# Optimization experiments

Hardware: AMD Instinct MI355X
Metric: run time of the kernel (lower is better)

Reference implementation:

```python
import jax, jax.numpy as jnp
import numpy as np

N = 100000  # nodes
E = 1600000  # edges
F = 128      # nfeat == nclass (source constructs every layer as nfeat->nclass)


def setup_inputs() -> dict:
    key = jax.random.key(0)
    ks = jax.random.split(key, 8)
    x = jax.random.normal(ks[0], (N, F), dtype=jnp.float32)
    row = jax.random.randint(ks[1], (E,), 0, N)
    col = jax.random.randint(ks[2], (E,), 0, N)
    s = (1.0 / np.sqrt(F)).astype(np.float32) if hasattr(1.0/np.sqrt(F), 'astype') else 1.0/np.sqrt(F)
    s = 1.0 / np.sqrt(F)
    W0 = jax.random.uniform(ks[3], (F, F), jnp.float32, -s, s)
    b0 = jax.random.uniform(ks[4], (F,), jnp.float32, -s, s)
    W1 = jax.random.uniform(ks[5], (F, F), jnp.float32, -s, s)
    b1 = jax.random.uniform(ks[6], (F,), jnp.float32, -s, s)
    return {"x": x, "W0": W0, "b0": b0, "W1": W1, "b1": b1, "row": row, "col": col}


def _gcn_layer(h_in, W, b, row, col, dinv):
    # h = Linear(feat)
    h = h_in @ W + b
    # (D^-1/2 (A+I) D^-1/2) @ h, A in COO (row=i, col=j), A[i,j]=1
    coef = dinv[row] * dinv[col]                      # [E]
    msg = h[col] * coef[:, None]                       # [E, F] gather
    agg = jax.ops.segment_sum(msg, row, num_segments=N)
    agg = agg + (dinv * dinv)[:, None] * h             # self loops (identity)
    return agg


def reference(x, W0, b0, W1, b1, row, col):
    # D_hat = diag((A + I).sum(0)) -> column sums + 1
    deg = jax.ops.segment_sum(jnp.ones((E,), jnp.float32), col, num_segments=N) + 1.0
    dinv = deg ** -0.5
    h = _gcn_layer(x, W0, b0, row, col, dinv)
    h = jax.nn.relu(h)            # with_relu=True; dropout off (eval mode)
    h = _gcn_layer(h, W1, b1, row, col, dinv)
    return jax.nn.log_softmax(h, axis=1)
```

## Files before the change

kernel.cpp:

```cpp
#include <hip/hip_runtime.h>
#include <math.h>

#define FDIM 128
#define RPB 128
#define BSTRIDE 32
#define NBLK 256
#define MAXB 1024

typedef __attribute__((ext_vector_type(8))) short short8;
typedef __attribute__((ext_vector_type(4))) float floatx4;

static __device__ __forceinline__ unsigned short f2bf(float f) {
    unsigned int u = __float_as_uint(f);
    u = (u + 0x7fff + ((u >> 16) & 1)) >> 16;
    return (unsigned short)u;
}

static __device__ __forceinline__ void bf2f(unsigned int u, float& a, float& b) {
    a = __uint_as_float(u << 16);
    b = __uint_as_float(u & 0xffff0000u);
}


__global__ __launch_bounds__(256) void k_zero(int* rbCnt, int* cbCnt, int nbs) {
    int i = blockIdx.x * 256 + threadIdx.x;
    if (i < nbs) { rbCnt[i] = 0; cbCnt[i] = 0; }
}

__global__ __launch_bounds__(256) void k_count(const int* __restrict__ row, const int* __restrict__ col,
                                               int* rbCnt, int* cbCnt, int nE, int nb) {
    __shared__ int rh[MAXB];
    __shared__ int ch[MAXB];
    const int tid = threadIdx.x;
    const int cpb = (nE + NBLK - 1) / NBLK;
    const int e0 = blockIdx.x * cpb;
    int e1 = e0 + cpb; if (e1 > nE) e1 = nE;
    for (int i = tid; i < nb; i += 256) { rh[i] = 0; ch[i] = 0; }
    __syncthreads();
    for (int e = e0 + tid; e < e1; e += 256) {
        atomicAdd(&rh[row[e] >> 7], 1);
        atomicAdd(&ch[col[e] >> 7], 1);
    }
    __syncthreads();
    for (int i = tid; i < nb; i += 256) {
        if (rh[i]) atomicAdd(&rbCnt[(size_t)i * BSTRIDE], rh[i]);
        if (ch[i]) atomicAdd(&cbCnt[(size_t)i * BSTRIDE], ch[i]);
    }
}

__global__ __launch_bounds__(1024) void k_bscan(const int* __restrict__ rbCnt, const int* __restrict__ cbCnt,
                                                int* rbBase, int* cbBase, int* rbCur, int* cbCur,
                                                int nb, int nE) {
    __shared__ int s[1024];
    int tid = threadIdx.x;
    int v = (tid < nb) ? rbCnt[(size_t)tid * BSTRIDE] : 0;
    s[tid] = v;
    __syncthreads();
    for (int off = 1; off < 1024; off <<= 1) {
        int t = (tid >= off) ? s[tid - off] : 0;
        __syncthreads();
        s[tid] += t;
        __syncthreads();
    }
    if (tid < nb) {
        int ex = s[tid] - v;
        rbBase[tid] = ex;
        rbCur[(size_t)tid * BSTRIDE] = ex;
    }
    if (tid == 0) rbBase[nb] = nE;
    __syncthreads();
    v = (tid < nb) ? cbCnt[(size_t)tid * BSTRIDE] : 0;
    s[tid] = v;
    __syncthreads();
    for (int off = 1; off < 1024; off <<= 1) {
        int t = (tid >= off) ? s[tid - off] : 0;
        __syncthreads();
        s[tid] += t;
        __syncthreads();
    }
    if (tid < nb) {
        int ex = s[tid] - v;
        cbBase[tid] = ex;
        cbCur[(size_t)tid * BSTRIDE] = ex;
    }
    if (tid == 0) cbBase[nb] = nE;
}

__global__ __launch_bounds__(256) void k_scatter2(const int* __restrict__ row, const int* __restrict__ col,
                                                  int* rbCur, int* cbCur,
                                                  unsigned int* __restrict__ pairs,
                                                  unsigned char* __restrict__ clocal, int nE, int nb) {
    __shared__ int rh[MAXB];
    __shared__ int ch[MAXB];
    __shared__ int rbase[MAXB];
    __shared__ int cbase[MAXB];
    const int tid = threadIdx.x;
    const int cpb = (nE + NBLK - 1) / NBLK;
    const int e0 = blockIdx.x * cpb;
    int e1 = e0 + cpb; if (e1 > nE) e1 = nE;

    for (int i = tid; i < nb; i += 256) { rh[i] = 0; ch[i] = 0; }
    __syncthreads();
    for (int e = e0 + tid; e < e1; e += 256) {
        atomicAdd(&rh[row[e] >> 7], 1);
        atomicAdd(&ch[col[e] >> 7], 1);
    }
    __syncthreads();
    for (int i = tid; i < nb; i += 256) {
        rbase[i] = rh[i] ? atomicAdd(&rbCur[(size_t)i * BSTRIDE], rh[i]) : 0;
        cbase[i] = ch[i] ? atomicAdd(&cbCur[(size_t)i * BSTRIDE], ch[i]) : 0;
        rh[i] = 0;
        ch[i] = 0;
    }
    __syncthreads();
    for (int e = e0 + tid; e < e1; e += 256) {
        int r = row[e];
        int c = col[e];
        int rb = r >> 7, cb = c >> 7;
        int p = rbase[rb] + atomicAdd(&rh[rb], 1);
        pairs[p] = ((unsigned int)(r & (RPB - 1)) << 25) | (unsigned int)c;
        int q = cbase[cb] + atomicAdd(&ch[cb], 1);
        clocal[q] = (unsigned char)(c & (RPB - 1));
    }
}

__global__ __launch_bounds__(256) void k_rowsort(const int* __restrict__ rbBase,
                                                 const unsigned int* __restrict__ pairs,
                                                 int* __restrict__ row_ptr, int* __restrict__ csr_col,
                                                 int n, int nb) {
    __shared__ int hist[RPB];
    __shared__ int scan[RPB];
    __shared__ int lcur[RPB];
    const int b = blockIdx.x;
    const int tid = threadIdx.x;
    const int row0 = b * RPB;
    const int start = rbBase[b];
    const int endp = rbBase[b + 1];

    if (tid < RPB) hist[tid] = 0;
    __syncthreads();
    for (int i = start + tid; i < endp; i += 256)
        atomicAdd(&hist[pairs[i] >> 25], 1);
    __syncthreads();

    if (tid < RPB) scan[tid] = hist[tid];
    __syncthreads();
    for (int off = 1; off < RPB; off <<= 1) {
        int t = (tid < RPB && tid >= off) ? scan[tid - off] : 0;
        __syncthreads();
        if (tid < RPB) scan[tid] += t;
        __syncthreads();
    }
    if (tid < RPB) {
        int ex = start + scan[tid] - hist[tid];
        lcur[tid] = ex;
        int r = row0 + tid;
        if (r < n) row_ptr[r] = ex;
    }
    if (b == nb - 1 && tid == 0) row_ptr[n] = endp;
    __syncthreads();

    for (int i = start + tid; i < endp; i += 256) {
        unsigned int u = pairs[i];
        int pos = atomicAdd(&lcur[u >> 25], 1);
        csr_col[pos] = (int)(u & 0x1FFFFFFu);
    }
}

__global__ __launch_bounds__(256) void k_colhist(const int* __restrict__ cbBase,
                                                 const unsigned char* __restrict__ clocal,
                                                 float* __restrict__ dinv, int n) {
    __shared__ int hist[RPB];
    const int b = blockIdx.x;
    const int tid = threadIdx.x;
    const int start = cbBase[b];
    const int endp = cbBase[b + 1];
    if (tid < RPB) hist[tid] = 0;
    __syncthreads();
    for (int i = start + tid; i < endp; i += 256)
        atomicAdd(&hist[(int)clocal[i]], 1);
    __syncthreads();
    if (tid < RPB) {
        int c = b * RPB + tid;
        if (c < n) dinv[c] = rsqrtf((float)hist[tid] + 1.0f);
    }
}


__global__ __launch_bounds__(256) void k_cvt(const float2* __restrict__ x, unsigned int* __restrict__ xb,
                                             int total) {
    int i = blockIdx.x * 256 + threadIdx.x;
    if (i < total) {
        float2 v = x[i];
        xb[i] = (unsigned int)f2bf(v.x) | ((unsigned int)f2bf(v.y) << 16);
    }
}

__global__ __launch_bounds__(256) void k_cvtW(const float* __restrict__ W0, const float* __restrict__ W1,
                                              unsigned short* __restrict__ W0t, unsigned short* __restrict__ W1t) {
    const float* W = blockIdx.x ? W1 : W0;
    unsigned short* Wt = blockIdx.x ? W1t : W0t;
    for (int idx = threadIdx.x; idx < FDIM * FDIM; idx += 256) {
        int k = idx >> 7, c = idx & 127;
        Wt[c * FDIM + k] = f2bf(W[idx]);
    }
}


#define KH 64
#define LPAD 72

__global__ __launch_bounds__(256) void k_gemm_mfma(const unsigned short* __restrict__ A,
                                                   const unsigned short* __restrict__ Wt,
                                                   const float* __restrict__ bias,
                                                   const float* __restrict__ dinv,
                                                   unsigned int* __restrict__ outp, int n) {
    __shared__ unsigned short sA[128][LPAD];
    __shared__ unsigned short sW[128][LPAD];

    const int tid = threadIdx.x;
    const int row0 = blockIdx.x * 128;
    const int wid = tid >> 6;
    const int lane = tid & 63;
    const int quad = lane >> 4;
    const int lq = lane & 15;
    const int wm = wid & 1;
    const int wn = wid >> 1;

    floatx4 acc[4][4];
#pragma unroll
    for (int i = 0; i < 4; i++)
#pragma unroll
        for (int j = 0; j < 4; j++) acc[i][j] = (floatx4){0.f, 0.f, 0.f, 0.f};

    for (int kh = 0; kh < 2; kh++) {
        if (kh) __syncthreads();
#pragma unroll
        for (int it = 0; it < 4; it++) {
            int f = tid + it * 256;
            int r = f >> 3;
            int c8 = (f & 7) * 8;
            int gr = row0 + r;
            uint4 v = make_uint4(0u, 0u, 0u, 0u);
            if (gr < n) v = *(const uint4*)&A[(size_t)gr * FDIM + kh * KH + c8];
            *(uint4*)&sA[r][c8] = v;
            uint4 wv = *(const uint4*)&Wt[(size_t)r * FDIM + kh * KH + c8];
            *(uint4*)&sW[r][c8] = wv;
        }
        __syncthreads();

#pragma unroll
        for (int kt = 0; kt < 2; kt++) {
            const int k0 = kt * 32 + quad * 8;
            short8 af[4], bf[4];
#pragma unroll
            for (int mt = 0; mt < 4; mt++)
                af[mt] = *(const short8*)&sA[wm * 64 + mt * 16 + lq][k0];
#pragma unroll
            for (int nt = 0; nt < 4; nt++)
                bf[nt] = *(const short8*)&sW[wn * 64 + nt * 16 + lq][k0];
#pragma unroll
            for (int mt = 0; mt < 4; mt++)
#pragma unroll
                for (int nt = 0; nt < 4; nt++)
                    acc[mt][nt] = __builtin_amdgcn_mfma_f32_16x16x32_bf16(af[mt], bf[nt], acc[mt][nt], 0, 0, 0);
        }
    }

    float bv[4];
#pragma unroll
    for (int nt = 0; nt < 4; nt++) bv[nt] = bias[wn * 64 + nt * 16 + lq];

#pragma unroll
    for (int mt = 0; mt < 4; mt++) {
#pragma unroll
        for (int r = 0; r < 4; r++) {
            int grow = row0 + wm * 64 + mt * 16 + quad * 4 + r;
            float di = (grow < n) ? dinv[grow] : 0.f;
#pragma unroll
            for (int nt = 0; nt < 4; nt++) {
                float v = (acc[mt][nt][r] + bv[nt]) * di;
                float pv = __shfl_xor(v, 1, 64);
                if (!(lq & 1) && grow < n) {
                    int col = wn * 64 + nt * 16 + lq;
                    outp[(size_t)grow * 64 + (col >> 1)] =
                        (unsigned int)f2bf(v) | ((unsigned int)f2bf(pv) << 16);
                }
            }
        }
    }
}


__global__ __launch_bounds__(256) void k_agg(const unsigned int* __restrict__ hs, const int* __restrict__ row_ptr,
                                             const int* __restrict__ csr_col, const float* __restrict__ dinv,
                                             void* __restrict__ out, int n, int relu, int lsm, int obf) {
    int w = (blockIdx.x * 256 + threadIdx.x) >> 6;
    int lane = threadIdx.x & 63;
    if (w >= n) return;
    float a0, a1;
    bf2f(hs[(size_t)w * 64 + lane], a0, a1);

    int e = row_ptr[w];
    const int end = row_ptr[w + 1];

    while (e < end) {
        int cnt = end - e;
        if (cnt > 64) cnt = 64;
        int jv = (e + lane < end) ? csr_col[e + lane] : 0;
        int t = 0;
        for (; t + 8 <= cnt; t += 8) {
            int j0 = __shfl(jv, t + 0, 64);
            int j1 = __shfl(jv, t + 1, 64);
            int j2 = __shfl(jv, t + 2, 64);
            int j3 = __shfl(jv, t + 3, 64);
            int j4 = __shfl(jv, t + 4, 64);
            int j5 = __shfl(jv, t + 5, 64);
            int j6 = __shfl(jv, t + 6, 64);
            int j7 = __shfl(jv, t + 7, 64);
            unsigned int u0 = hs[(size_t)j0 * 64 + lane];
            unsigned int u1 = hs[(size_t)j1 * 64 + lane];
            unsigned int u2 = hs[(size_t)j2 * 64 + lane];
            unsigned int u3 = hs[(size_t)j3 * 64 + lane];
            unsigned int u4 = hs[(size_t)j4 * 64 + lane];
            unsigned int u5 = hs[(size_t)j5 * 64 + lane];
            unsigned int u6 = hs[(size_t)j6 * 64 + lane];
            unsigned int u7 = hs[(size_t)j7 * 64 + lane];
            float x0, y0, x1, y1, x2, y2, x3, y3, x4, y4, x5, y5, x6, y6, x7, y7;
            bf2f(u0, x0, y0); bf2f(u1, x1, y1); bf2f(u2, x2, y2); bf2f(u3, x3, y3);
            bf2f(u4, x4, y4); bf2f(u5, x5, y5); bf2f(u6, x6, y6); bf2f(u7, x7, y7);
            a0 += ((x0 + x1) + (x2 + x3)) + ((x4 + x5) + (x6 + x7));
            a1 += ((y0 + y1) + (y2 + y3)) + ((y4 + y5) + (y6 + y7));
        }
        for (; t < cnt; t++) {
            int j = __shfl(jv, t, 64);
            float ux, uy;
            bf2f(hs[(size_t)j * 64 + lane], ux, uy);
            a0 += ux;
            a1 += uy;
        }
        e += cnt;
    }

    float di = dinv[w];
    a0 *= di;
    a1 *= di;
    if (relu) {
        a0 = fmaxf(a0, 0.0f);
        a1 = fmaxf(a1, 0.0f);
    }
    if (lsm) {
        float m = fmaxf(a0, a1);
#pragma unroll
        for (int off = 32; off > 0; off >>= 1) m = fmaxf(m, __shfl_xor(m, off, 64));
        float s = expf(a0 - m) + expf(a1 - m);
#pragma unroll
        for (int off = 32; off > 0; off >>= 1) s += __shfl_xor(s, off, 64);
        float lg = m + logf(s);
        a0 -= lg;
        a1 -= lg;
    }
    if (obf) {
        ((unsigned int*)out)[(size_t)w * 64 + lane] =
            (unsigned int)f2bf(a0) | ((unsigned int)f2bf(a1) << 16);
    } else {
        ((float2*)out)[(size_t)w * 64 + lane] = make_float2(a0, a1);
    }
}


extern "C" void kernel_launch(void* const* d_in, const int* in_sizes, int n_in,
                              void* d_out, int out_size, void* d_ws, size_t ws_size,
                              hipStream_t stream) {
    const float* x  = (const float*)d_in[0];
    const float* W0 = (const float*)d_in[1];
    const float* b0 = (const float*)d_in[2];
    const float* W1 = (const float*)d_in[3];
    const float* b1 = (const float*)d_in[4];
    const int* row  = (const int*)d_in[5];
    const int* col  = (const int*)d_in[6];
    float* out = (float*)d_out;

    const int N = in_sizes[0] / FDIM;
    const int E = in_sizes[5];
    const int NB = (N + RPB - 1) / RPB;

    char* w = (char*)d_ws;
    size_t off = 0;
    auto alloc = [&](size_t bytes) {
        char* p = w + off;
        off += (bytes + 255) & ~(size_t)255;
        return p;
    };
    int* rbCnt   = (int*)alloc((size_t)NB * BSTRIDE * 4);
    int* cbCnt   = (int*)alloc((size_t)NB * BSTRIDE * 4);
    int* rbCur   = (int*)alloc((size_t)NB * BSTRIDE * 4);
    int* cbCur   = (int*)alloc((size_t)NB * BSTRIDE * 4);
    int* rbBase  = (int*)alloc((size_t)(NB + 1) * 4);
    int* cbBase  = (int*)alloc((size_t)(NB + 1) * 4);
    float* dinv  = (float*)alloc((size_t)N * 4);
    int* row_ptr = (int*)alloc((size_t)(N + 1) * 4);
    int* csr_col = (int*)alloc((size_t)E * 4);
    unsigned short* W0t = (unsigned short*)alloc((size_t)FDIM * FDIM * 2);
    unsigned short* W1t = (unsigned short*)alloc((size_t)FDIM * FDIM * 2);
    unsigned int* hs = (unsigned int*)alloc((size_t)N * 64 * 4);
    size_t uniSz = (size_t)E * 4 + (size_t)E + 512;
    size_t xbSz  = (size_t)N * 64 * 4;
    char* uni = (char*)alloc(uniSz > xbSz ? uniSz : xbSz);
    unsigned int* pairs = (unsigned int*)uni;
    unsigned char* clocal = (unsigned char*)uni + (size_t)E * 4;
    unsigned int* xb = (unsigned int*)uni;
    unsigned int* hb = (unsigned int*)uni;

    const int gW = (N * 64 + 255) / 256;
    const int gG = (N + 127) / 128;
    const int gZ = (NB * BSTRIDE + 255) / 256;
    const int gC = (N * 64 + 255) / 256;

    k_zero<<<gZ, 256, 0, stream>>>(rbCnt, cbCnt, NB * BSTRIDE);
    k_count<<<NBLK, 256, 0, stream>>>(row, col, rbCnt, cbCnt, E, NB);
    k_bscan<<<1, 1024, 0, stream>>>(rbCnt, cbCnt, rbBase, cbBase, rbCur, cbCur, NB, E);
    k_scatter2<<<NBLK, 256, 0, stream>>>(row, col, rbCur, cbCur, pairs, clocal, E, NB);
    k_rowsort<<<NB, 256, 0, stream>>>(rbBase, pairs, row_ptr, csr_col, N, NB);
    k_colhist<<<NB, 256, 0, stream>>>(cbBase, clocal, dinv, N);

    k_cvtW<<<2, 256, 0, stream>>>(W0, W1, W0t, W1t);
    k_cvt<<<gC, 256, 0, stream>>>((const float2*)x, xb, N * 64);

    k_gemm_mfma<<<gG, 256, 0, stream>>>((const unsigned short*)xb, W0t, b0, dinv, hs, N);
    k_agg<<<gW, 256, 0, stream>>>(hs, row_ptr, csr_col, dinv, hb, N, 1, 0, 1);

    k_gemm_mfma<<<gG, 256, 0, stream>>>((const unsigned short*)hb, W1t, b1, dinv, hs, N);
    k_agg<<<gW, 256, 0, stream>>>(hs, row_ptr, csr_col, dinv, out, N, 0, 1, 0);
}
```

Before: 410.2 us.

## Fuse fp32-to-bf16 input conversion into GEMM and pad gather with zero row

Removes the separate x conversion kernel by loading fp32 x directly in the first GEMM and packing to bf16 with the hardware pack instruction. The aggregation loop now gathers 16 neighbours per step using readlane, and out-of-range slots point at an appended zero row of hs. This drops the scalar tail loop. It saves a full read and write pass over x and shortens the gather inner loop, at the cost of wasted loads on padded slots for low-degree rows. Rounding may differ slightly from the manual f2bf path.

After: 397.5 us. 3.1% less time.

```diff
diff --git a/kernel.cpp b/kernel.cpp
--- a/kernel.cpp
+++ b/kernel.cpp
@@ -16,15 +16,22 @@
     return (unsigned short)u;
 }
 
+static __device__ __forceinline__ unsigned int cvtpk(float a, float b) {
+    unsigned int r;
+    asm("v_cvt_pk_bf16_f32 %0, %1, %2" : "=v"(r) : "v"(a), "v"(b));
+    return r;
+}
+
 static __device__ __forceinline__ void bf2f(unsigned int u, float& a, float& b) {
     a = __uint_as_float(u << 16);
     b = __uint_as_float(u & 0xffff0000u);
 }
 
 
-__global__ __launch_bounds__(256) void k_zero(int* rbCnt, int* cbCnt, int nbs) {
+__global__ __launch_bounds__(256) void k_zero(int* rbCnt, int* cbCnt, int nbs, unsigned int* hsz) {
     int i = blockIdx.x * 256 + threadIdx.x;
     if (i < nbs) { rbCnt[i] = 0; cbCnt[i] = 0; }
+    if (blockIdx.x == 0 && threadIdx.x < 64) hsz[threadIdx.x] = 0u;
 }
 
 __global__ __launch_bounds__(256) void k_count(const int* __restrict__ row, const int* __restrict__ col,
@@ -187,15 +194,6 @@
 }
 
 
-__global__ __launch_bounds__(256) void k_cvt(const float2* __restrict__ x, unsigned int* __restrict__ xb,
-                                             int total) {
-    int i = blockIdx.x * 256 + threadIdx.x;
-    if (i < total) {
-        float2 v = x[i];
-        xb[i] = (unsigned int)f2bf(v.x) | ((unsigned int)f2bf(v.y) << 16);
-    }
-}
-
 __global__ __launch_bounds__(256) void k_cvtW(const float* __restrict__ W0, const float* __restrict__ W1,
                                               unsigned short* __restrict__ W0t, unsigned short* __restrict__ W1t) {
     const float* W = blockIdx.x ? W1 : W0;
@@ -210,13 +208,16 @@
 #define KH 64
 #define LPAD 72
 
-__global__ __launch_bounds__(256) void k_gemm_mfma(const unsigned short* __restrict__ A,
+__global__ __launch_bounds__(256) void k_gemm_mfma(const void* __restrict__ Ain,
                                                    const unsigned short* __restrict__ Wt,
                                                    const float* __restrict__ bias,
                                                    const float* __restrict__ dinv,
-                                                   unsigned int* __restrict__ outp, int n) {
+                                                   unsigned int* __restrict__ outp, int n, int af32) {
     __shared__ unsigned short sA[128][LPAD];
     __shared__ unsigned short sW[128][LPAD];
+
+    const unsigned short* A = (const unsigned short*)Ain;
+    const float* Af = (const float*)Ain;
 
     const int tid = threadIdx.x;
     const int row0 = blockIdx.x * 128;
@@ -241,9 +242,24 @@
             int r = f >> 3;
             int c8 = (f & 7) * 8;
             int gr = row0 + r;
-            uint4 v = make_uint4(0u, 0u, 0u, 0u);
-            if (gr < n) v = *(const uint4*)&A[(size_t)gr * FDIM + kh * KH + c8];
-            *(uint4*)&sA[r][c8] = v;
+            if (af32) {
+                float4 v0 = make_float4(0.f, 0.f, 0.f, 0.f);
+                float4 v1 = make_float4(0.f, 0.f, 0.f, 0.f);
+                if (gr < n) {
+                    v0 = *(const float4*)&Af[(size_t)gr * FDIM + kh * KH + c8];
+                    v1 = *(const float4*)&Af[(size_t)gr * FDIM + kh * KH + c8 + 4];
+                }
+                uint4 p;
+                p.x = cvtpk(v0.x, v0.y);
+                p.y = cvtpk(v0.z, v0.w);
+                p.z = cvtpk(v1.x, v1.y);
+                p.w = cvtpk(v1.z, v1.w);
+                *(uint4*)&sA[r][c8] = p;
+            } else {
+                uint4 v = make_uint4(0u, 0u, 0u, 0u);
+                if (gr < n) v = *(const uint4*)&A[(size_t)gr * FDIM + kh * KH + c8];
+                *(uint4*)&sA[r][c8] = v;
+            }
             uint4 wv = *(const uint4*)&Wt[(size_t)r * FDIM + kh * KH + c8];
             *(uint4*)&sW[r][c8] = wv;
         }
@@ -292,6 +308,9 @@
 }
 
 
+#define GATH(i) int j##i = __builtin_amdgcn_readlane(jv, t + i); \
+                unsigned int u##i = hs[(size_t)j##i * 64 + lane];
+
 __global__ __launch_bounds__(256) void k_agg(const unsigned int* __restrict__ hs, const int* __restrict__ row_ptr,
                                              const int* __restrict__ csr_col, const float* __restrict__ dinv,
                                              void* __restrict__ out, int n, int relu, int lsm, int obf) {
@@ -303,41 +322,27 @@
 
     int e = row_ptr[w];
     const int end = row_ptr[w + 1];
+    const int zrow = n;
 
     while (e < end) {
         int cnt = end - e;
         if (cnt > 64) cnt = 64;
-        int jv = (e + lane < end) ? csr_col[e + lane] : 0;
-        int t = 0;
-        for (; t + 8 <= cnt; t += 8) {
-            int j0 = __shfl(jv, t + 0, 64);
-            int j1 = __shfl(jv, t + 1, 64);
-            int j2 = __shfl(jv, t + 2, 64);
-            int j3 = __shfl(jv, t + 3, 64);
-            int j4 = __shfl(jv, t + 4, 64);
-            int j5 = __shfl(jv, t + 5, 64);
-            int j6 = __shfl(jv, t + 6, 64);
-            int j7 = __shfl(jv, t + 7, 64);
-            unsigned int u0 = hs[(size_t)j0 * 64 + lane];
-            unsigned int u1 = hs[(size_t)j1 * 64 + lane];
-            unsigned int u2 = hs[(size_t)j2 * 64 + lane];
-            unsigned int u3 = hs[(size_t)j3 * 64 + lane];
-            unsigned int u4 = hs[(size_t)j4 * 64 + lane];
-            unsigned int u5 = hs[(size_t)j5 * 64 + lane];
-            unsigned int u6 = hs[(size_t)j6 * 64 + lane];
-            unsigned int u7 = hs[(size_t)j7 * 64 + lane];
+        int jv = (e + lane < end) ? csr_col[e + lane] : zrow;
+        for (int t = 0; t < cnt; t += 16) {
+            GATH(0)  GATH(1)  GATH(2)  GATH(3)
+            GATH(4)  GATH(5)  GATH(6)  GATH(7)
+            GATH(8)  GATH(9)  GATH(10) GATH(11)
+            GATH(12) GATH(13) GATH(14) GATH(15)
             float x0, y0, x1, y1, x2, y2, x3, y3, x4, y4, x5, y5, x6, y6, x7, y7;
-            bf2f(u0, x0, y0); bf2f(u1, x1, y1); bf2f(u2, x2, y2); bf2f(u3, x3, y3);
-            bf2f(u4, x4, y4); bf2f(u5, x5, y5); bf2f(u6, x6, y6); bf2f(u7, x7, y7);
-            a0 += ((x0 + x1) + (x2 + x3)) + ((x4 + x5) + (x6 + x7));
-            a1 += ((y0 + y1) + (y2 + y3)) + ((y4 + y5) + (y6 + y7));
-        }
-        for (; t < cnt; t++) {
-            int j = __shfl(jv, t, 64);
-            float ux, uy;
-            bf2f(hs[(size_t)j * 64 + lane], ux, uy);
-            a0 += ux;
-            a1 += uy;
+            float x8, y8, x9, y9, x10, y10, x11, y11, x12, y12, x13, y13, x14, y14, x15, y15;
+            bf2f(u0, x0, y0);   bf2f(u1, x1, y1);   bf2f(u2, x2, y2);   bf2f(u3, x3, y3);
+            bf2f(u4, x4, y4);   bf2f(u5, x5, y5);   bf2f(u6, x6, y6);   bf2f(u7, x7, y7);
+            bf2f(u8, x8, y8);   bf2f(u9, x9, y9);   bf2f(u10, x10, y10); bf2f(u11, x11, y11);
+            bf2f(u12, x12, y12); bf2f(u13, x13, y13); bf2f(u14, x14, y14); bf2f(u15, x15, y15);
+            a0 += ((((x0 + x1) + (x2 + x3)) + ((x4 + x5) + (x6 + x7))) +
+                   (((x8 + x9) + (x10 + x11)) + ((x12 + x13) + (x14 + x15))));
+            a1 += ((((y0 + y1) + (y2 + y3)) + ((y4 + y5) + (y6 + y7))) +
+                   (((y8 + y9) + (y10 + y11)) + ((y12 + y13) + (y14 + y15))));
         }
         e += cnt;
     }
@@ -403,21 +408,19 @@
     int* csr_col = (int*)alloc((size_t)E * 4);
     unsigned short* W0t = (unsigned short*)alloc((size_t)FDIM * FDIM * 2);
     unsigned short* W1t = (unsigned short*)alloc((size_t)FDIM * FDIM * 2);
-    unsigned int* hs = (unsigned int*)alloc((size_t)N * 64 * 4);
+    unsigned int* hs = (unsigned int*)alloc((size_t)(N + 1) * 64 * 4);
     size_t uniSz = (size_t)E * 4 + (size_t)E + 512;
-    size_t xbSz  = (size_t)N * 64 * 4;
-    char* uni = (char*)alloc(uniSz > xbSz ? uniSz : xbSz);
+    size_t hbSz  = (size_t)N * 64 * 4;
+    char* uni = (char*)alloc(uniSz > hbSz ? uniSz : hbSz);
     unsigned int* pairs = (unsigned int*)uni;
     unsigned char* clocal = (unsigned char*)uni + (size_t)E * 4;
-    unsigned int* xb = (unsigned int*)uni;
     unsigned int* hb = (unsigned int*)uni;
 
     const int gW = (N * 64 + 255) / 256;
     const int gG = (N + 127) / 128;
     const int gZ = (NB * BSTRIDE + 255) / 256;
-    const int gC = (N * 64 + 255) / 256;
-
-    k_zero<<<gZ, 256, 0, stream>>>(rbCnt, cbCnt, NB * BSTRIDE);
+
+    k_zero<<<gZ, 256, 0, stream>>>(rbCnt, cbCnt, NB * BSTRIDE, hs + (size_t)N * 64);
     k_count<<<NBLK, 256, 0, stream>>>(row, col, rbCnt, cbCnt, E, NB);
     k_bscan<<<1, 1024, 0, stream>>>(rbCnt, cbCnt, rbBase, cbBase, rbCur, cbCur, NB, E);
     k_scatter2<<<NBLK, 256, 0, stream>>>(row, col, rbCur, cbCur, pairs, clocal, E, NB);
@@ -425,11 +428,10 @@
     k_colhist<<<NB, 256, 0, stream>>>(cbBase, clocal, dinv, N);
 
     k_cvtW<<<2, 256, 0, stream>>>(W0, W1, W0t, W1t);
-    k_cvt<<<gC, 256, 0, stream>>>((const float2*)x, xb, N * 64);
-
-    k_gemm_mfma<<<gG, 256, 0, stream>>>((const unsigned short*)xb, W0t, b0, dinv, hs, N);
+
+    k_gemm_mfma<<<gG, 256, 0, stream>>>((const void*)x, W0t, b0, dinv, hs, N, 1);
     k_agg<<<gW, 256, 0, stream>>>(hs, row_ptr, csr_col, dinv, hb, N, 1, 0, 1);
 
-    k_gemm_mfma<<<gG, 256, 0, stream>>>((const unsigned short*)hb, W1t, b1, dinv, hs, N);
+    k_gemm_mfma<<<gG, 256, 0, stream>>>((const void*)hb, W1t, b1, dinv, hs, N, 0);
     k_agg<<<gW, 256, 0, stream>>>(hs, row_ptr, csr_col, dinv, out, N, 0, 1, 0);
 }
```
